# Optimization experiments

Measured on AMD Instinct MI355X. Metric: run time of the kernel, lower is better.

The kernel has to match this reference:

```python
import jax, jax.numpy as jnp
import numpy as np
from jax import lax

WIN = 9
PAD = WIN // 2
DIM = 3
WIN_VOL = WIN ** DIM  # 729
EPS_DENOM = 1e-05


def _box_sum(x):
    # x: (N, 1, D, H, W); all-ones WINxWINxWIN box filter, 'same' padding
    kernel = jnp.ones((1, 1, WIN, WIN, WIN), dtype=x.dtype)
    return lax.conv_general_dilated(
        x, kernel,
        window_strides=(1, 1, 1),
        padding=[(PAD, PAD)] * 3,
        dimension_numbers=("NCDHW", "OIDHW", "NCDHW"),
    )


def setup_inputs() -> dict:
    key = jax.random.key(0)
    k1, k2 = jax.random.split(key)
    shape = (2, 1, 160, 192, 160)
    I = jax.random.uniform(k1, shape, dtype=jnp.float32)
    J = jax.random.uniform(k2, shape, dtype=jnp.float32)
    return {"I": I, "J": J}


def reference(I, J):
    n = I.shape[0]
    # Fuse the five box-filter convs into one by stacking along the batch dim
    stacked = jnp.concatenate([I, J, I * I, J * J, I * J], axis=0)
    sums = _box_sum(stacked)
    I_sum, J_sum, I2_sum, J2_sum, IJ_sum = (
        sums[0 * n:1 * n], sums[1 * n:2 * n], sums[2 * n:3 * n],
        sums[3 * n:4 * n], sums[4 * n:5 * n],
    )
    wv = jnp.asarray(WIN_VOL, dtype=I.dtype)
    E_I = I_sum / wv
    E_J = J_sum / wv
    cross = IJ_sum - I_sum * E_J - J_sum * E_I + E_I * E_J * wv
    I_var = I2_sum - 2 * E_I * I_sum + E_I * E_I * wv
    J_var = J2_sum - 2 * E_J * J_sum + E_J * E_J * wv
    cc = cross * cross / (I_var * J_var + EPS_DENOM)
    return -jnp.mean(cc)
```

## Files before the change

### kernel.cpp

```cpp
#include <hip/hip_runtime.h>


namespace {
constexpr int Wd = 160, Hd = 192, Dd = 160, NB = 2;
constexpr long DSTRIDE = (long)Hd * Wd;
constexpr long VOLUME  = (long)Dd * DSTRIDE;
constexpr int BW = 32, BH = 12, BD = 19;
constexpr int EH = BH + 8;
constexpr int NWB = 5, NHB = 16, NDB = 9;
constexpr int NBLK = NB * NDB * NHB * NWB;
constexpr int NT = 384;
constexpr int CH  = EH * BW;
constexpr int HWC = BH * BW;
constexpr int NPLANES = BD + 8;
constexpr float INV_WV = 1.0f / 729.0f;
constexpr float NEG_INV_TOTAL = -1.0f / 9830400.0f;
}

__device__ __forceinline__ void bar_lds() {
    asm volatile("s_waitcnt lgkmcnt(0)\n\ts_barrier" ::: "memory");
}

__device__ __forceinline__ float4 slide9(float v0, float v1, float v2, float v3,
                                         float v4, float v5, float v6, float v7,
                                         float v8, float v9, float v10, float v11) {
    float s8 = ((v0 + v1) + (v2 + v3)) + ((v4 + v5) + (v6 + v7)) + v8;
    float4 o;
    o.x = s8;
    o.y = o.x + (v9 - v0);
    o.z = o.y + (v10 - v1);
    o.w = o.z + (v11 - v2);
    return o;
}

__global__ __launch_bounds__(NT) void k_ncc(const float* __restrict__ I,
                                            const float* __restrict__ J,
                                            float* __restrict__ out) {
    __shared__ float ws[5 * CH];
    __shared__ float hw[5 * HWC];
    __shared__ float red[NT];

    const int tid = threadIdx.x;
    int bx = blockIdx.x;
    const int wb = bx % NWB; bx /= NWB;
    const int hb = bx % NHB; bx /= NHB;
    const int db = bx % NDB; bx /= NDB;
    const int n  = bx;
    const int w0 = wb * BW, h0 = hb * BH, d0 = db * BD;
    const long nvol = (long)n * VOLUME;

    const int seg = tid & 7;
    const int yy  = tid >> 3;
    const bool aJob = (tid < 160);
    const int ah    = h0 - 4 + yy;
    const int wbase = w0 - 4 + (seg << 2);
    const bool ahOk = aJob && ((unsigned)ah < (unsigned)Hd);
    const bool qok0 = ((unsigned)(wbase + 0) < (unsigned)Wd);
    const bool qok1 = ((unsigned)(wbase + 4) < (unsigned)Wd);
    const bool qok2 = ((unsigned)(wbase + 8) < (unsigned)Wd);
    const long roff = nvol + (long)ah * Wd + wbase + (long)(d0 - 4) * DSTRIDE;
    const float* aI = I + roff;
    const float* aJ = J + roff;

    const int c2 = tid >> 4;
    const int wp = tid & 15;
    const float2* const a2src = (const float2*)(ws + c2 * CH) + wp;
    float2* const a2dst = (float2*)(hw + c2 * HWC) + wp;

    const int tx = tid & 31, ty = tid >> 5;

    float4 pI0, pI1, pI2, pJ0, pJ1, pJ2;

#define ISSUE(PP)                                                            \
    do {                                                                     \
        const bool _pv = ahOk && ((unsigned)(PP) < (unsigned)Dd);            \
        pI0 = (_pv && qok0) ? *(const float4*)(aI + 0) : float4{0, 0, 0, 0}; \
        pI1 = (_pv && qok1) ? *(const float4*)(aI + 4) : float4{0, 0, 0, 0}; \
        pI2 = (_pv && qok2) ? *(const float4*)(aI + 8) : float4{0, 0, 0, 0}; \
        pJ0 = (_pv && qok0) ? *(const float4*)(aJ + 0) : float4{0, 0, 0, 0}; \
        pJ1 = (_pv && qok1) ? *(const float4*)(aJ + 4) : float4{0, 0, 0, 0}; \
        pJ2 = (_pv && qok2) ? *(const float4*)(aJ + 8) : float4{0, 0, 0, 0}; \
    } while (0)

    float hist[9][5];
#pragma unroll
    for (int k = 0; k < 9; ++k)
#pragma unroll
        for (int c = 0; c < 5; ++c) hist[k][c] = 0.0f;
    float sa[5] = {0, 0, 0, 0, 0};
    float acc = 0.0f;

    ISSUE(d0 - 4);

#pragma unroll 1
    for (int M = 0; M < 3; ++M) {
#pragma unroll
        for (int u = 0; u < 9; ++u) {
            const int t = 9 * M + u;
            const int p = d0 - 4 + t;
            const bool pvalid = ((unsigned)p < (unsigned)Dd);

            if (pvalid && aJob) {
                const float a0 = pI0.x, a1 = pI0.y, a2 = pI0.z, a3 = pI0.w;
                const float a4 = pI1.x, a5 = pI1.y, a6 = pI1.z, a7 = pI1.w;
                const float a8 = pI2.x, a9 = pI2.y, a10 = pI2.z, a11 = pI2.w;
                const float b0 = pJ0.x, b1 = pJ0.y, b2 = pJ0.z, b3 = pJ0.w;
                const float b4 = pJ1.x, b5 = pJ1.y, b6 = pJ1.z, b7 = pJ1.w;
                const float b8 = pJ2.x, b9 = pJ2.y, b10 = pJ2.z, b11 = pJ2.w;
                float* const wab = ws + yy * BW + (seg << 2);
                *(float4*)(wab + 0 * CH) =
                    slide9(a0, a1, a2, a3, a4, a5, a6, a7, a8, a9, a10, a11);
                *(float4*)(wab + 1 * CH) =
                    slide9(b0, b1, b2, b3, b4, b5, b6, b7, b8, b9, b10, b11);
                *(float4*)(wab + 2 * CH) =
                    slide9(a0 * a0, a1 * a1, a2 * a2, a3 * a3, a4 * a4, a5 * a5,
                           a6 * a6, a7 * a7, a8 * a8, a9 * a9, a10 * a10, a11 * a11);
                *(float4*)(wab + 3 * CH) =
                    slide9(b0 * b0, b1 * b1, b2 * b2, b3 * b3, b4 * b4, b5 * b5,
                           b6 * b6, b7 * b7, b8 * b8, b9 * b9, b10 * b10, b11 * b11);
                *(float4*)(wab + 4 * CH) =
                    slide9(a0 * b0, a1 * b1, a2 * b2, a3 * b3, a4 * b4, a5 * b5,
                           a6 * b6, a7 * b7, a8 * b8, a9 * b9, a10 * b10, a11 * b11);
            }
            aI += DSTRIDE; aJ += DSTRIDE;
            if (t < NPLANES - 1) { ISSUE(p + 1); }

            bar_lds();

            if (pvalid && tid < 80) {
                const float2* const src = a2src;
                float2* const dst = a2dst;
                float2 g0 = src[0 * 16], g1 = src[1 * 16];
                float2 g2 = src[2 * 16], g3 = src[3 * 16];
                float2 g4 = src[4 * 16], g5 = src[5 * 16];
                float2 g6 = src[6 * 16], g7 = src[7 * 16];
                float2 s;
                s.x = ((g0.x + g1.x) + (g2.x + g3.x)) + ((g4.x + g5.x) + (g6.x + g7.x));
                s.y = ((g0.y + g1.y) + (g2.y + g3.y)) + ((g4.y + g5.y) + (g6.y + g7.y));
                float2 r, h8, h9, h10;
                r = src[ 8 * 16]; h8 = r;
                s.x += r.x; s.y += r.y; dst[ 0 * 16] = s; s.x -= g0.x; s.y -= g0.y;
                r = src[ 9 * 16]; h9 = r;
                s.x += r.x; s.y += r.y; dst[ 1 * 16] = s; s.x -= g1.x; s.y -= g1.y;
                r = src[10 * 16]; h10 = r;
                s.x += r.x; s.y += r.y; dst[ 2 * 16] = s; s.x -= g2.x; s.y -= g2.y;
                r = src[11 * 16];
                s.x += r.x; s.y += r.y; dst[ 3 * 16] = s; s.x -= g3.x; s.y -= g3.y;
                r = src[12 * 16];
                s.x += r.x; s.y += r.y; dst[ 4 * 16] = s; s.x -= g4.x; s.y -= g4.y;
                r = src[13 * 16];
                s.x += r.x; s.y += r.y; dst[ 5 * 16] = s; s.x -= g5.x; s.y -= g5.y;
                r = src[14 * 16];
                s.x += r.x; s.y += r.y; dst[ 6 * 16] = s; s.x -= g6.x; s.y -= g6.y;
                r = src[15 * 16];
                s.x += r.x; s.y += r.y; dst[ 7 * 16] = s; s.x -= g7.x; s.y -= g7.y;
                r = src[16 * 16];
                s.x += r.x; s.y += r.y; dst[ 8 * 16] = s; s.x -= h8.x; s.y -= h8.y;
                r = src[17 * 16];
                s.x += r.x; s.y += r.y; dst[ 9 * 16] = s; s.x -= h9.x; s.y -= h9.y;
                r = src[18 * 16];
                s.x += r.x; s.y += r.y; dst[10 * 16] = s; s.x -= h10.x; s.y -= h10.y;
                r = src[19 * 16];
                s.x += r.x; s.y += r.y; dst[11 * 16] = s;
            }

            bar_lds();

            float h5[5];
            if (pvalid) {
#pragma unroll
                for (int c = 0; c < 5; ++c)
                    h5[c] = hw[c * HWC + ty * BW + tx];
            } else {
#pragma unroll
                for (int c = 0; c < 5; ++c) h5[c] = 0.0f;
            }
#pragma unroll
            for (int c = 0; c < 5; ++c) sa[c] += h5[c];
            const int dout = d0 + t - 8;
            if (t >= 8 && dout < Dd) {
                const float cross = sa[4] - sa[0] * sa[1] * INV_WV;
                const float iv    = sa[2] - sa[0] * sa[0] * INV_WV;
                const float jv    = sa[3] - sa[1] * sa[1] * INV_WV;
                acc += (cross * cross) * __builtin_amdgcn_rcpf(iv * jv + 1e-5f);
            }
#pragma unroll
            for (int c = 0; c < 5; ++c) sa[c] -= hist[(u + 1) % 9][c];
#pragma unroll
            for (int c = 0; c < 5; ++c) hist[u][c] = h5[c];
        }
    }
#undef ISSUE

    red[tid] = acc;
    __syncthreads();
    if (tid < 128) red[tid] += red[tid + 256];
    __syncthreads();
    for (int off = 128; off > 0; off >>= 1) {
        if (tid < off) red[tid] += red[tid + off];
        __syncthreads();
    }
    if (tid == 0) atomicAdd(out, red[0] * NEG_INV_TOTAL);
}

extern "C" void kernel_launch(void* const* d_in, const int* in_sizes, int n_in,
                              void* d_out, int out_size, void* d_ws, size_t ws_size,
                              hipStream_t stream) {
    const float* I = (const float*)d_in[0];
    const float* J = (const float*)d_in[1];
    float* out = (float*)d_out;

    hipMemsetAsync(d_out, 0, sizeof(float), stream);
    k_ncc<<<NBLK, NT, 0, stream>>>(I, J, out);
}
```

Before: 184.9 us.

## Split box filter into W/H pass with fp16 workspace plus separate depth pass

Adds a two-kernel path. The first kernel computes the W and H box sums for all five channels with no depth halo and stores them as packed fp16 in the workspace. The second kernel slides along depth per column, reading that fp16 data, and reduces the NCC. This removes the 8-plane depth halo recompute of the fused kernel, at the cost of a round trip through global memory and fp16 rounding of sums that can reach around 81. A retiled fused kernel with 512 threads is kept as a fallback for when the workspace is too small.

```diff
diff --git a/kernel.cpp b/kernel.cpp
--- a/kernel.cpp
+++ b/kernel.cpp
@@ -1,21 +1,34 @@
 #include <hip/hip_runtime.h>
+#include <hip/hip_fp16.h>
 
 
 namespace {
 constexpr int Wd = 160, Hd = 192, Dd = 160, NB = 2;
 constexpr long DSTRIDE = (long)Hd * Wd;
 constexpr long VOLUME  = (long)Dd * DSTRIDE;
-constexpr int BW = 32, BH = 12, BD = 19;
-constexpr int EH = BH + 8;
-constexpr int NWB = 5, NHB = 16, NDB = 9;
-constexpr int NBLK = NB * NDB * NHB * NWB;
-constexpr int NT = 384;
-constexpr int CH  = EH * BW;
-constexpr int HWC = BH * BW;
-constexpr int NPLANES = BD + 8;
+constexpr long TOTAL   = VOLUME * NB;
 constexpr float INV_WV = 1.0f / 729.0f;
 constexpr float NEG_INV_TOTAL = -1.0f / 9830400.0f;
-}
+
+constexpr int BW1 = 32, BH1 = 24, EH1 = 32, DC1 = 8;
+constexpr int WT1 = 5, HT1 = 8, NDC1 = 20;
+constexpr int NBLK1 = NB * NDC1 * HT1 * WT1;
+constexpr int CH1 = EH1 * BW1;
+
+constexpr int DK2 = 19, NCH2 = 9;
+constexpr int NBLK2 = (int)((long)NB * NCH2 * Hd * Wd / 256);
+
+constexpr int BWf = 32, BHf = 16, EHf = 24;
+constexpr int NWBf = 5, NHBf = 12, NDBf = 9;
+constexpr int NBLKf = NB * NDBf * NHBf * NWBf;
+constexpr int CHf  = EHf * BWf;
+constexpr int HWCf = BHf * BWf;
+constexpr int NPLf = 27;
+
+constexpr size_t WS_NEEDED = (size_t)5 * (size_t)TOTAL * 2;
+}
+
+typedef _Float16 half2v __attribute__((ext_vector_type(2)));
 
 __device__ __forceinline__ void bar_lds() {
     asm volatile("s_waitcnt lgkmcnt(0)\n\ts_barrier" ::: "memory");
@@ -33,25 +46,211 @@
     return o;
 }
 
-__global__ __launch_bounds__(NT) void k_ncc(const float* __restrict__ I,
+__device__ __forceinline__ unsigned int pk32(float lo, float hi) {
+    half2v h = (half2v)__builtin_amdgcn_cvt_pkrtz(lo, hi);
+    return __builtin_bit_cast(unsigned int, h);
+}
+
+__global__ __launch_bounds__(256) void k_wh(const float* __restrict__ I,
                                             const float* __restrict__ J,
-                                            float* __restrict__ out) {
-    __shared__ float ws[5 * CH];
-    __shared__ float hw[5 * HWC];
-    __shared__ float red[NT];
+                                            unsigned int* __restrict__ hwOut) {
+    __shared__ float ws[5 * CH1];
 
     const int tid = threadIdx.x;
     int bx = blockIdx.x;
-    const int wb = bx % NWB; bx /= NWB;
-    const int hb = bx % NHB; bx /= NHB;
-    const int db = bx % NDB; bx /= NDB;
+    const int wt = bx % WT1; bx /= WT1;
+    const int ht = bx % HT1; bx /= HT1;
+    const int dc = bx % NDC1; bx /= NDC1;
     const int n  = bx;
-    const int w0 = wb * BW, h0 = hb * BH, d0 = db * BD;
+    const int w0 = wt * BW1, h0 = ht * BH1, d0 = dc * DC1;
     const long nvol = (long)n * VOLUME;
 
     const int seg = tid & 7;
     const int yy  = tid >> 3;
-    const bool aJob = (tid < 160);
+    const int ah  = h0 - 4 + yy;
+    const int wbase = w0 - 4 + (seg << 2);
+    const bool ahOk = ((unsigned)ah < (unsigned)Hd);
+    const bool qok0 = ((unsigned)(wbase + 0) < (unsigned)Wd);
+    const bool qok1 = ((unsigned)(wbase + 4) < (unsigned)Wd);
+    const bool qok2 = ((unsigned)(wbase + 8) < (unsigned)Wd);
+    const float* aI = I + nvol + (long)ah * Wd + wbase + (long)d0 * DSTRIDE;
+    const float* aJ = J + nvol + (long)ah * Wd + wbase + (long)d0 * DSTRIDE;
+
+    const int c2 = tid >> 5;
+    const int h2 = (tid >> 4) & 1;
+    const int wp = tid & 15;
+    const float2* const a2src = (const float2*)(ws + c2 * CH1) + (h2 * 12) * 16 + wp;
+    long obase = ((long)c2 * TOTAL + nvol + (long)d0 * DSTRIDE
+                  + (long)(h0 + h2 * 12) * Wd + w0) / 2 + wp;
+
+    float4 pI0, pI1, pI2, pJ0, pJ1, pJ2;
+
+#define ISSUE()                                                             \
+    do {                                                                    \
+        pI0 = (ahOk && qok0) ? *(const float4*)(aI + 0) : float4{0, 0, 0, 0}; \
+        pI1 = (ahOk && qok1) ? *(const float4*)(aI + 4) : float4{0, 0, 0, 0}; \
+        pI2 = (ahOk && qok2) ? *(const float4*)(aI + 8) : float4{0, 0, 0, 0}; \
+        pJ0 = (ahOk && qok0) ? *(const float4*)(aJ + 0) : float4{0, 0, 0, 0}; \
+        pJ1 = (ahOk && qok1) ? *(const float4*)(aJ + 4) : float4{0, 0, 0, 0}; \
+        pJ2 = (ahOk && qok2) ? *(const float4*)(aJ + 8) : float4{0, 0, 0, 0}; \
+    } while (0)
+
+    ISSUE();
+
+#pragma unroll 1
+    for (int pp = 0; pp < DC1; ++pp) {
+        {
+            const float a0 = pI0.x, a1 = pI0.y, a2 = pI0.z, a3 = pI0.w;
+            const float a4 = pI1.x, a5 = pI1.y, a6 = pI1.z, a7 = pI1.w;
+            const float a8 = pI2.x, a9 = pI2.y, a10 = pI2.z, a11 = pI2.w;
+            const float b0 = pJ0.x, b1 = pJ0.y, b2 = pJ0.z, b3 = pJ0.w;
+            const float b4 = pJ1.x, b5 = pJ1.y, b6 = pJ1.z, b7 = pJ1.w;
+            const float b8 = pJ2.x, b9 = pJ2.y, b10 = pJ2.z, b11 = pJ2.w;
+            float* const wab = ws + yy * BW1 + (seg << 2);
+            *(float4*)(wab + 0 * CH1) =
+                slide9(a0, a1, a2, a3, a4, a5, a6, a7, a8, a9, a10, a11);
+            *(float4*)(wab + 1 * CH1) =
+                slide9(b0, b1, b2, b3, b4, b5, b6, b7, b8, b9, b10, b11);
+            *(float4*)(wab + 2 * CH1) =
+                slide9(a0 * a0, a1 * a1, a2 * a2, a3 * a3, a4 * a4, a5 * a5,
+                       a6 * a6, a7 * a7, a8 * a8, a9 * a9, a10 * a10, a11 * a11);
+            *(float4*)(wab + 3 * CH1) =
+                slide9(b0 * b0, b1 * b1, b2 * b2, b3 * b3, b4 * b4, b5 * b5,
+                       b6 * b6, b7 * b7, b8 * b8, b9 * b9, b10 * b10, b11 * b11);
+            *(float4*)(wab + 4 * CH1) =
+                slide9(a0 * b0, a1 * b1, a2 * b2, a3 * b3, a4 * b4, a5 * b5,
+                       a6 * b6, a7 * b7, a8 * b8, a9 * b9, a10 * b10, a11 * b11);
+        }
+        aI += DSTRIDE; aJ += DSTRIDE;
+        if (pp < DC1 - 1) { ISSUE(); }
+
+        bar_lds();
+
+        if (tid < 160) {
+            const float2* const src = a2src;
+            unsigned int* const o = hwOut + obase;
+            float2 g0 = src[0 * 16], g1 = src[1 * 16];
+            float2 g2 = src[2 * 16], g3 = src[3 * 16];
+            float2 g4 = src[4 * 16], g5 = src[5 * 16];
+            float2 g6 = src[6 * 16], g7 = src[7 * 16];
+            float2 s;
+            s.x = ((g0.x + g1.x) + (g2.x + g3.x)) + ((g4.x + g5.x) + (g6.x + g7.x));
+            s.y = ((g0.y + g1.y) + (g2.y + g3.y)) + ((g4.y + g5.y) + (g6.y + g7.y));
+            float2 r, h8, h9, h10;
+            r = src[ 8 * 16]; h8 = r;
+            s.x += r.x; s.y += r.y; o[ 0 * 80] = pk32(s.x, s.y); s.x -= g0.x; s.y -= g0.y;
+            r = src[ 9 * 16]; h9 = r;
+            s.x += r.x; s.y += r.y; o[ 1 * 80] = pk32(s.x, s.y); s.x -= g1.x; s.y -= g1.y;
+            r = src[10 * 16]; h10 = r;
+            s.x += r.x; s.y += r.y; o[ 2 * 80] = pk32(s.x, s.y); s.x -= g2.x; s.y -= g2.y;
+            r = src[11 * 16];
+            s.x += r.x; s.y += r.y; o[ 3 * 80] = pk32(s.x, s.y); s.x -= g3.x; s.y -= g3.y;
+            r = src[12 * 16];
+            s.x += r.x; s.y += r.y; o[ 4 * 80] = pk32(s.x, s.y); s.x -= g4.x; s.y -= g4.y;
+            r = src[13 * 16];
+            s.x += r.x; s.y += r.y; o[ 5 * 80] = pk32(s.x, s.y); s.x -= g5.x; s.y -= g5.y;
+            r = src[14 * 16];
+            s.x += r.x; s.y += r.y; o[ 6 * 80] = pk32(s.x, s.y); s.x -= g6.x; s.y -= g6.y;
+            r = src[15 * 16];
+            s.x += r.x; s.y += r.y; o[ 7 * 80] = pk32(s.x, s.y); s.x -= g7.x; s.y -= g7.y;
+            r = src[16 * 16];
+            s.x += r.x; s.y += r.y; o[ 8 * 80] = pk32(s.x, s.y); s.x -= h8.x; s.y -= h8.y;
+            r = src[17 * 16];
+            s.x += r.x; s.y += r.y; o[ 9 * 80] = pk32(s.x, s.y); s.x -= h9.x; s.y -= h9.y;
+            r = src[18 * 16];
+            s.x += r.x; s.y += r.y; o[10 * 80] = pk32(s.x, s.y); s.x -= h10.x; s.y -= h10.y;
+            r = src[19 * 16];
+            s.x += r.x; s.y += r.y; o[11 * 80] = pk32(s.x, s.y);
+        }
+        obase += DSTRIDE / 2;
+
+        bar_lds();
+    }
+#undef ISSUE
+}
+
+__global__ __launch_bounds__(256) void k_dcc(const unsigned short* __restrict__ hwIn,
+                                             float* __restrict__ out) {
+    const int tid = threadIdx.x;
+    long gid = (long)blockIdx.x * 256 + tid;
+    const int w = (int)(gid % Wd); gid /= Wd;
+    const int h = (int)(gid % Hd); gid /= Hd;
+    const int ck = (int)(gid % NCH2); gid /= NCH2;
+    const int n = (int)gid;
+    const int d0 = ck * DK2;
+    const long cbase = (long)n * VOLUME + (long)h * Wd + w;
+
+    float hist[9][5];
+#pragma unroll
+    for (int k = 0; k < 9; ++k)
+#pragma unroll
+        for (int c = 0; c < 5; ++c) hist[k][c] = 0.0f;
+    float sa[5] = {0, 0, 0, 0, 0};
+    float acc = 0.0f;
+
+#pragma unroll 1
+    for (int M = 0; M < 3; ++M) {
+#pragma unroll
+        for (int u = 0; u < 9; ++u) {
+            const int t = 9 * M + u;
+            const int p = d0 - 4 + t;
+            float h5[5];
+            if ((unsigned)p < (unsigned)Dd) {
+                const long idx = cbase + (long)p * DSTRIDE;
+#pragma unroll
+                for (int c = 0; c < 5; ++c) {
+                    const unsigned short v = hwIn[idx + (long)c * TOTAL];
+                    h5[c] = (float)__builtin_bit_cast(_Float16, v);
+                }
+            } else {
+#pragma unroll
+                for (int c = 0; c < 5; ++c) h5[c] = 0.0f;
+            }
+#pragma unroll
+            for (int c = 0; c < 5; ++c) sa[c] += h5[c];
+            const int dout = d0 + t - 8;
+            if (t >= 8 && dout < Dd) {
+                const float cross = sa[4] - sa[0] * sa[1] * INV_WV;
+                const float iv    = sa[2] - sa[0] * sa[0] * INV_WV;
+                const float jv    = sa[3] - sa[1] * sa[1] * INV_WV;
+                acc += (cross * cross) * __builtin_amdgcn_rcpf(iv * jv + 1e-5f);
+            }
+#pragma unroll
+            for (int c = 0; c < 5; ++c) sa[c] -= hist[(u + 1) % 9][c];
+#pragma unroll
+            for (int c = 0; c < 5; ++c) hist[u][c] = h5[c];
+        }
+    }
+
+    __shared__ float red[256];
+    red[tid] = acc;
+    __syncthreads();
+    for (int off = 128; off > 0; off >>= 1) {
+        if (tid < off) red[tid] += red[tid + off];
+        __syncthreads();
+    }
+    if (tid == 0) atomicAdd(out, red[0] * NEG_INV_TOTAL);
+}
+
+__global__ __launch_bounds__(512) void k_fused(const float* __restrict__ I,
+                                               const float* __restrict__ J,
+                                               float* __restrict__ out) {
+    __shared__ float ws[5 * CHf];
+    __shared__ float hw[5 * HWCf];
+    __shared__ float red[512];
+
+    const int tid = threadIdx.x;
+    int bx = blockIdx.x;
+    const int wb = bx % NWBf; bx /= NWBf;
+    const int hb = bx % NHBf; bx /= NHBf;
+    const int db = bx % NDBf; bx /= NDBf;
+    const int n  = bx;
+    const int w0 = wb * BWf, h0 = hb * BHf, d0 = db * 19;
+    const long nvol = (long)n * VOLUME;
+
+    const int seg = tid & 7;
+    const int yy  = tid >> 3;
+    const bool aJob = (tid < 192);
     const int ah    = h0 - 4 + yy;
     const int wbase = w0 - 4 + (seg << 2);
     const bool ahOk = aJob && ((unsigned)ah < (unsigned)Hd);
@@ -62,16 +261,17 @@
     const float* aI = I + roff;
     const float* aJ = J + roff;
 
-    const int c2 = tid >> 4;
+    const int c2 = tid >> 5;
     const int wp = tid & 15;
-    const float2* const a2src = (const float2*)(ws + c2 * CH) + wp;
-    float2* const a2dst = (float2*)(hw + c2 * HWC) + wp;
+    const int hq = (tid >> 4) & 1;
+    const float2* const a2src = (const float2*)(ws + c2 * CHf) + (hq * 8) * 16 + wp;
+    float2* const a2dst = (float2*)(hw + c2 * HWCf) + (hq * 8) * 16 + wp;
 
     const int tx = tid & 31, ty = tid >> 5;
 
     float4 pI0, pI1, pI2, pJ0, pJ1, pJ2;
 
-#define ISSUE(PP)                                                            \
+#define ISSUEF(PP)                                                           \
     do {                                                                     \
         const bool _pv = ahOk && ((unsigned)(PP) < (unsigned)Dd);            \
         pI0 = (_pv && qok0) ? *(const float4*)(aI + 0) : float4{0, 0, 0, 0}; \
@@ -90,7 +290,7 @@
     float sa[5] = {0, 0, 0, 0, 0};
     float acc = 0.0f;
 
-    ISSUE(d0 - 4);
+    ISSUEF(d0 - 4);
 
 #pragma unroll 1
     for (int M = 0; M < 3; ++M) {
@@ -107,61 +307,45 @@
                 const float b0 = pJ0.x, b1 = pJ0.y, b2 = pJ0.z, b3 = pJ0.w;
                 const float b4 = pJ1.x, b5 = pJ1.y, b6 = pJ1.z, b7 = pJ1.w;
                 const float b8 = pJ2.x, b9 = pJ2.y, b10 = pJ2.z, b11 = pJ2.w;
-                float* const wab = ws + yy * BW + (seg << 2);
-                *(float4*)(wab + 0 * CH) =
+                float* const wab = ws + yy * BWf + (seg << 2);
+                *(float4*)(wab + 0 * CHf) =
                     slide9(a0, a1, a2, a3, a4, a5, a6, a7, a8, a9, a10, a11);
-                *(float4*)(wab + 1 * CH) =
+                *(float4*)(wab + 1 * CHf) =
                     slide9(b0, b1, b2, b3, b4, b5, b6, b7, b8, b9, b10, b11);
-                *(float4*)(wab + 2 * CH) =
+                *(float4*)(wab + 2 * CHf) =
                     slide9(a0 * a0, a1 * a1, a2 * a2, a3 * a3, a4 * a4, a5 * a5,
                            a6 * a6, a7 * a7, a8 * a8, a9 * a9, a10 * a10, a11 * a11);
-                *(float4*)(wab + 3 * CH) =
+                *(float4*)(wab + 3 * CHf) =
                     slide9(b0 * b0, b1 * b1, b2 * b2, b3 * b3, b4 * b4, b5 * b5,
                            b6 * b6, b7 * b7, b8 * b8, b9 * b9, b10 * b10, b11 * b11);
-                *(float4*)(wab + 4 * CH) =
+                *(float4*)(wab + 4 * CHf) =
                     slide9(a0 * b0, a1 * b1, a2 * b2, a3 * b3, a4 * b4, a5 * b5,
                            a6 * b6, a7 * b7, a8 * b8, a9 * b9, a10 * b10, a11 * b11);
             }
             aI += DSTRIDE; aJ += DSTRIDE;
-            if (t < NPLANES - 1) { ISSUE(p + 1); }
+            if (t < 26) { ISSUEF(p + 1); }
 
             bar_lds();
 
-            if (pvalid && tid < 80) {
+            if (pvalid && tid < 160) {
                 const float2* const src = a2src;
                 float2* const dst = a2dst;
-                float2 g0 = src[0 * 16], g1 = src[1 * 16];
-                float2 g2 = src[2 * 16], g3 = src[3 * 16];
-                float2 g4 = src[4 * 16], g5 = src[5 * 16];
-                float2 g6 = src[6 * 16], g7 = src[7 * 16];
+                const float2 g0 = src[0 * 16], g1 = src[1 * 16];
+                const float2 g2 = src[2 * 16], g3 = src[3 * 16];
+                const float2 g4 = src[4 * 16], g5 = src[5 * 16];
+                const float2 g6 = src[6 * 16], g7 = src[7 * 16];
                 float2 s;
                 s.x = ((g0.x + g1.x) + (g2.x + g3.x)) + ((g4.x + g5.x) + (g6.x + g7.x));
                 s.y = ((g0.y + g1.y) + (g2.y + g3.y)) + ((g4.y + g5.y) + (g6.y + g7.y));
-                float2 r, h8, h9, h10;
-                r = src[ 8 * 16]; h8 = r;
-                s.x += r.x; s.y += r.y; dst[ 0 * 16] = s; s.x -= g0.x; s.y -= g0.y;
-                r = src[ 9 * 16]; h9 = r;
-                s.x += r.x; s.y += r.y; dst[ 1 * 16] = s; s.x -= g1.x; s.y -= g1.y;
-                r = src[10 * 16]; h10 = r;
-                s.x += r.x; s.y += r.y; dst[ 2 * 16] = s; s.x -= g2.x; s.y -= g2.y;
-                r = src[11 * 16];
-                s.x += r.x; s.y += r.y; dst[ 3 * 16] = s; s.x -= g3.x; s.y -= g3.y;
-                r = src[12 * 16];
-                s.x += r.x; s.y += r.y; dst[ 4 * 16] = s; s.x -= g4.x; s.y -= g4.y;
-                r = src[13 * 16];
-                s.x += r.x; s.y += r.y; dst[ 5 * 16] = s; s.x -= g5.x; s.y -= g5.y;
-                r = src[14 * 16];
-                s.x += r.x; s.y += r.y; dst[ 6 * 16] = s; s.x -= g6.x; s.y -= g6.y;
-                r = src[15 * 16];
-                s.x += r.x; s.y += r.y; dst[ 7 * 16] = s; s.x -= g7.x; s.y -= g7.y;
-                r = src[16 * 16];
-                s.x += r.x; s.y += r.y; dst[ 8 * 16] = s; s.x -= h8.x; s.y -= h8.y;
-                r = src[17 * 16];
-                s.x += r.x; s.y += r.y; dst[ 9 * 16] = s; s.x -= h9.x; s.y -= h9.y;
-                r = src[18 * 16];
-                s.x += r.x; s.y += r.y; dst[10 * 16] = s; s.x -= h10.x; s.y -= h10.y;
-                r = src[19 * 16];
-                s.x += r.x; s.y += r.y; dst[11 * 16] = s;
+                float2 r;
+                r = src[ 8 * 16]; s.x += r.x; s.y += r.y; dst[0 * 16] = s; s.x -= g0.x; s.y -= g0.y;
+                r = src[ 9 * 16]; s.x += r.x; s.y += r.y; dst[1 * 16] = s; s.x -= g1.x; s.y -= g1.y;
+                r = src[10 * 16]; s.x += r.x; s.y += r.y; dst[2 * 16] = s; s.x -= g2.x; s.y -= g2.y;
+                r = src[11 * 16]; s.x += r.x; s.y += r.y; dst[3 * 16] = s; s.x -= g3.x; s.y -= g3.y;
+                r = src[12 * 16]; s.x += r.x; s.y += r.y; dst[4 * 16] = s; s.x -= g4.x; s.y -= g4.y;
+                r = src[13 * 16]; s.x += r.x; s.y += r.y; dst[5 * 16] = s; s.x -= g5.x; s.y -= g5.y;
+                r = src[14 * 16]; s.x += r.x; s.y += r.y; dst[6 * 16] = s; s.x -= g6.x; s.y -= g6.y;
+                r = src[15 * 16]; s.x += r.x; s.y += r.y; dst[7 * 16] = s;
             }
 
             bar_lds();
@@ -170,7 +354,7 @@
             if (pvalid) {
 #pragma unroll
                 for (int c = 0; c < 5; ++c)
-                    h5[c] = hw[c * HWC + ty * BW + tx];
+                    h5[c] = hw[c * HWCf + ty * BWf + tx];
             } else {
 #pragma unroll
                 for (int c = 0; c < 5; ++c) h5[c] = 0.0f;
@@ -190,13 +374,11 @@
             for (int c = 0; c < 5; ++c) hist[u][c] = h5[c];
         }
     }
-#undef ISSUE
+#undef ISSUEF
 
     red[tid] = acc;
     __syncthreads();
-    if (tid < 128) red[tid] += red[tid + 256];
-    __syncthreads();
-    for (int off = 128; off > 0; off >>= 1) {
+    for (int off = 256; off > 0; off >>= 1) {
         if (tid < off) red[tid] += red[tid + off];
         __syncthreads();
     }
@@ -211,5 +393,10 @@
     float* out = (float*)d_out;
 
     hipMemsetAsync(d_out, 0, sizeof(float), stream);
-    k_ncc<<<NBLK, NT, 0, stream>>>(I, J, out);
-}
+    if (ws_size >= WS_NEEDED) {
+        k_wh<<<NBLK1, 256, 0, stream>>>(I, J, (unsigned int*)d_ws);
+        k_dcc<<<NBLK2, 256, 0, stream>>>((const unsigned short*)d_ws, out);
+    } else {
+        k_fused<<<NBLKf, 512, 0, stream>>>(I, J, out);
+    }
+}
```

Result: slower. 196.4 us (+6.2%).
